# Optimization experiments

Measured on AMD Instinct MI355X. Metric: run time of the kernel, lower is better.

The kernel has to match this reference:

```python
import jax, jax.numpy as jnp
import numpy as np

VOCAB = 50257
D_MODEL = 256
HIDDEN = 512
NUM_CLASSES = 2
BATCH = 64
SEQ = 512
PAD_IDX = 0


def setup_inputs() -> dict:
    key = jax.random.key(0)
    ks = jax.random.split(key, 8)
    input_ids = jax.random.randint(ks[0], (BATCH, SEQ), 0, VOCAB)
    emb = jax.random.normal(ks[1], (VOCAB, D_MODEL), dtype=jnp.float32) * 0.02
    emb = emb.at[PAD_IDX].set(0.0)  # padding_idx row is zero
    s_x = 1.0 / np.sqrt(D_MODEL)
    s_h = 1.0 / np.sqrt(HIDDEN)
    Wx = jax.random.uniform(ks[2], (D_MODEL, 3 * HIDDEN), minval=-s_x, maxval=s_x)
    Wh = jax.random.uniform(ks[3], (HIDDEN, 3 * HIDDEN), minval=-s_h, maxval=s_h)
    bx = jax.random.uniform(ks[4], (3 * HIDDEN,), minval=-s_h, maxval=s_h)
    bh = jax.random.uniform(ks[5], (3 * HIDDEN,), minval=-s_h, maxval=s_h)
    Wo = jax.random.uniform(ks[6], (HIDDEN, NUM_CLASSES), minval=-s_h, maxval=s_h)
    bo = jax.random.uniform(ks[7], (NUM_CLASSES,), minval=-s_h, maxval=s_h)
    return {"input_ids": input_ids, "emb": emb, "Wx": Wx, "Wh": Wh,
            "bx": bx, "bh": bh, "Wo": Wo, "bo": bo}


def reference(input_ids, emb, Wx, Wh, bx, bh, Wo, bo):
    # Embedding lookup: [B, S, D]
    x = emb[input_ids]
    # Precompute input-side gate projections for all timesteps: [B, S, 3H]
    xg = jnp.einsum('bsd,dg->bsg', x, Wx) + bx
    H = Wh.shape[0]
    h0 = jnp.zeros((input_ids.shape[0], H), dtype=x.dtype)

    def step(h, xg_t):
        hg = h @ Wh + bh                    # [B, 3H]
        xr, xz, xn = jnp.split(xg_t, 3, axis=-1)
        hr, hz, hn = jnp.split(hg, 3, axis=-1)
        r = jax.nn.sigmoid(xr + hr)
        z = jax.nn.sigmoid(xz + hz)
        n = jnp.tanh(xn + r * hn)
        h_new = (1.0 - z) * n + z * h
        return h_new, None

    # scan over time; only the last hidden state feeds the classifier head
    h_last, _ = jax.lax.scan(step, h0, jnp.swapaxes(xg, 0, 1))
    # Dropout is identity in eval mode (p=0.5 at train time)
    logits = h_last @ Wo + bo               # [B, num_classes]
    return logits
```

## Files before the change

kernel.cpp:

```cpp
#include <hip/hip_runtime.h>
#include <hip/hip_bf16.h>

#define BATCH   64
#define SEQ     512
#define DMODEL  256
#define HIDDEN  512
#define G3      1536
#define NBLK    128
#define UPB     4
#define CPB     12
#define CHUNK   128
#define NCHUNK  4
#define HSLOT   (HIDDEN * BATCH)

typedef unsigned long long u64;
typedef unsigned int u32;

__global__ __launch_bounds__(512) void prep_wh(const float* __restrict__ Wh,
                                               float* __restrict__ whp) {
    int t = blockIdx.x * 512 + threadIdx.x;
    int k   = t & 511;
    int cb  = t >> 9;
    int c   = cb % 12;
    int blk = cb / 12;
    int u = c & 3, g = c >> 2;
    whp[t] = Wh[(long)k * G3 + g * HIDDEN + blk * UPB + u];
}

__global__ void init_flags(unsigned* flags) {
    __hip_atomic_store(&flags[threadIdx.x], 0u, __ATOMIC_RELAXED,
                       __HIP_MEMORY_SCOPE_AGENT);
}

__global__ __launch_bounds__(256) void xg_gemm(const int* __restrict__ ids,
                                               const float* __restrict__ emb,
                                               const float* __restrict__ Wx,
                                               const float* __restrict__ bx,
                                               float* __restrict__ xgC,
                                               int chunk) {
    __shared__ float Es[64][68];
    __shared__ float Ws[64][68];
    __shared__ int   sids[64];

    const int tid = threadIdx.x;
    const int nb = blockIdx.x;
    const int lt = blockIdx.y;
    const int s  = chunk * CHUNK + lt;
    const int tn = tid & 15;
    const int tm = tid >> 4;

    if (tid < 64) sids[tid] = ids[tid * SEQ + s];
    __syncthreads();

    float acc[4][4];
#pragma unroll
    for (int i = 0; i < 4; ++i)
#pragma unroll
        for (int j = 0; j < 4; ++j) acc[i][j] = 0.f;

    for (int kb = 0; kb < 256; kb += 64) {
#pragma unroll
        for (int p = 0; p < 4; ++p) {
            int b = p * 16 + tm;
            float4 av = *(const float4*)(emb + (long)sids[b] * DMODEL + kb + tn * 4);
            Es[tn * 4 + 0][b] = av.x;
            Es[tn * 4 + 1][b] = av.y;
            Es[tn * 4 + 2][b] = av.z;
            Es[tn * 4 + 3][b] = av.w;
            int krow = p * 16 + tm;
            float4 wv = *(const float4*)(Wx + (long)(kb + krow) * G3 + nb * 64 + tn * 4);
            *(float4*)&Ws[krow][tn * 4] = wv;
        }
        __syncthreads();
#pragma unroll
        for (int k = 0; k < 64; ++k) {
            float4 w4 = *(const float4*)&Ws[k][tm * 4];
            float4 e4 = *(const float4*)&Es[k][tn * 4];
            float ww[4] = {w4.x, w4.y, w4.z, w4.w};
            float ee[4] = {e4.x, e4.y, e4.z, e4.w};
#pragma unroll
            for (int i = 0; i < 4; ++i)
#pragma unroll
                for (int j = 0; j < 4; ++j)
                    acc[i][j] = fmaf(ww[i], ee[j], acc[i][j]);
        }
        __syncthreads();
    }

#pragma unroll
    for (int i = 0; i < 4; ++i) {
        int col = nb * 64 + tm * 4 + i;
        float bxi = bx[col];
        float4 o;
        o.x = acc[i][0] + bxi;
        o.y = acc[i][1] + bxi;
        o.z = acc[i][2] + bxi;
        o.w = acc[i][3] + bxi;
        *(float4*)(xgC + (long)col * (CHUNK * BATCH) + lt * 64 + tn * 4) = o;
    }
}

__global__ __launch_bounds__(512, 2) void gru_scan(const float* __restrict__ whp,
                                                   const float* __restrict__ xgC,
                                                   const float* __restrict__ bh,
                                                   float* hist,
                                                   unsigned* flags,
                                                   int chunk) {
    const int tid = threadIdx.x;
    const int blk = blockIdx.x;
    const int b   = tid & 63;
    const int wu  = __builtin_amdgcn_readfirstlane(tid >> 6);

    __shared__ float part[2][8][CPB][64];

    const float* wb = whp + blk * (CPB * HIDDEN) + wu * 64;
    const int base = chunk * CHUNK;

    int jg = 0;
    float bhr = 0.f, bhz = 0.f, bhn = 0.f, hprev = 0.f;
    const float* xr_p = nullptr; const float* xz_p = nullptr; const float* xn_p = nullptr;
    if (wu < 4) {
        jg  = blk * UPB + wu;
        bhr = bh[jg];
        bhz = bh[HIDDEN + jg];
        bhn = bh[2 * HIDDEN + jg];
        xr_p = xgC + (long)jg * (CHUNK * BATCH) + b;
        xz_p = xgC + (long)(HIDDEN + jg) * (CHUNK * BATCH) + b;
        xn_p = xgC + (long)(2 * HIDDEN + jg) * (CHUNK * BATCH) + b;
        hprev = (chunk == 0) ? 0.f : hist[(long)jg * 64 + b];
    }

#pragma unroll 1
    for (int lt = 0; lt < CHUNK; ++lt) {
        const int t  = base + lt;
        const int pb = lt & 1;
        const float* hs = hist + (long)lt * HSLOT;
        float*       hw = hist + (long)((lt + 1) & (CHUNK - 1)) * HSLOT;

        float xr = 0.f, xz = 0.f, xn = 0.f;
        if (wu < 4) {
            xr = xr_p[lt * 64];
            xz = xz_p[lt * 64];
            xn = xn_p[lt * 64];
        }

        float acc[CPB];
#pragma unroll
        for (int c = 0; c < CPB; ++c) acc[c] = 0.f;

        if (t > 0) {
            if (lt > 0) {
                const u32 tgt = (u32)t;
                for (;;) {
                    u32 f = __hip_atomic_load(&flags[wu * 64 + b], __ATOMIC_RELAXED,
                                              __HIP_MEMORY_SCOPE_AGENT);
                    if (__all((int)(f >= tgt))) break;
                    __builtin_amdgcn_s_sleep(1);
                }
            }
            const float* hq = hs + (long)wu * (64 * 64) + b;
            float hv[64];
#pragma unroll
            for (int i = 0; i < 64; ++i)
                hv[i] = hq[i * 64];

#pragma unroll
            for (int i = 0; i < 64; ++i) {
                const float hvv = hv[i];
#pragma unroll
                for (int c = 0; c < CPB; ++c)
                    acc[c] = fmaf(hvv, wb[c * HIDDEN + i], acc[c]);
            }
        }

#pragma unroll
        for (int c = 0; c < CPB; ++c) part[pb][wu][c][b] = acc[c];
        __syncthreads();

        if (wu < 4) {
            __builtin_amdgcn_s_setprio(1);
            float hgr = bhr, hgz = bhz, hgn = bhn;
#pragma unroll
            for (int ww = 0; ww < 8; ++ww) {
                hgr += part[pb][ww][wu][b];
                hgz += part[pb][ww][4 + wu][b];
                hgn += part[pb][ww][8 + wu][b];
            }
            float r  = 1.f / (1.f + expf(-(xr + hgr)));
            float z  = 1.f / (1.f + expf(-(xz + hgz)));
            float nn = tanhf(xn + r * hgn);
            float hnew = (1.f - z) * nn + z * hprev;
            hprev = hnew;
            __hip_atomic_store((u32*)hw + (long)jg * 64 + b, __float_as_uint(hnew),
                               __ATOMIC_RELAXED, __HIP_MEMORY_SCOPE_AGENT);
            asm volatile("s_waitcnt vmcnt(0)" ::: "memory");
            if (b == 0)
                __hip_atomic_store(&flags[jg], (u32)(t + 1), __ATOMIC_RELAXED,
                                   __HIP_MEMORY_SCOPE_AGENT);
            __builtin_amdgcn_s_setprio(0);
        }
    }
}

__global__ void head_kernel(const float* __restrict__ hist,
                            const float* __restrict__ Wo,
                            const float* __restrict__ bo,
                            float* __restrict__ out) {
    int tid = threadIdx.x;
    int b = tid >> 1, n = tid & 1;
    float acc = bo[n];
#pragma unroll 8
    for (int k = 0; k < HIDDEN; ++k)
        acc = fmaf(hist[(long)k * 64 + b], Wo[k * 2 + n], acc);
    out[b * 2 + n] = acc;
}

extern "C" void kernel_launch(void* const* d_in, const int* in_sizes, int n_in,
                              void* d_out, int out_size, void* d_ws, size_t ws_size,
                              hipStream_t stream) {
    (void)in_sizes; (void)n_in; (void)out_size; (void)ws_size;
    const int*   ids = (const int*)  d_in[0];
    const float* emb = (const float*)d_in[1];
    const float* Wx  = (const float*)d_in[2];
    const float* Wh  = (const float*)d_in[3];
    const float* bx  = (const float*)d_in[4];
    const float* bh  = (const float*)d_in[5];
    const float* Wo  = (const float*)d_in[6];
    const float* bo  = (const float*)d_in[7];
    float* out = (float*)d_out;

    char* ws = (char*)d_ws;
    unsigned* flags = (unsigned*)ws;
    float* hist = (float*)(ws + 2048);
    float* whp  = (float*)(ws + 2048 + (size_t)CHUNK * HSLOT * 4);
    float* xgC  = (float*)(ws + 2048 + (size_t)CHUNK * HSLOT * 4
                           + (size_t)NBLK * CPB * HIDDEN * 4);

    init_flags<<<dim3(1), dim3(512), 0, stream>>>(flags);
    prep_wh<<<dim3(1536), dim3(512), 0, stream>>>(Wh, whp);
    for (int c = 0; c < NCHUNK; ++c) {
        xg_gemm<<<dim3(24, CHUNK), dim3(256), 0, stream>>>(ids, emb, Wx, bx, xgC, c);
        gru_scan<<<dim3(NBLK), dim3(512), 0, stream>>>(whp, xgC, bh, hist, flags, c);
    }
    head_kernel<<<dim3(1), dim3(128), 0, stream>>>(hist, Wo, bo, out);
}
```

Measured before the change: 5.683 ms.

## Replace per-step flag handshake with NaN-sentinel polling on hidden-state data

Drops the separate flags array and the per-step store-wait-then-flag-publish protocol in the GRU scan. Consumers now poll the hidden-state slots directly with atomic loads until no value equals a NaN sentinel, and a new kernel refills the history buffer with sentinels before each chunk. This removes one dependent global-memory round trip per timestep from the serial critical path. In exchange it adds a 16 MB clear per chunk and busy-spinning full 64-value reloads without sleep, and it assumes the real hidden state never takes the sentinel bit pattern.

```diff
diff --git a/kernel.cpp b/kernel.cpp
--- a/kernel.cpp
+++ b/kernel.cpp
@@ -13,6 +13,9 @@
 #define NCHUNK  4
 #define HSLOT   (HIDDEN * BATCH)
 
+#define SENT32  0xFFC00000u
+#define SENT64  0xFFC00000FFC00000ULL
+
 typedef unsigned long long u64;
 typedef unsigned int u32;
 
@@ -27,9 +30,10 @@
     whp[t] = Wh[(long)k * G3 + g * HIDDEN + blk * UPB + u];
 }
 
-__global__ void init_flags(unsigned* flags) {
-    __hip_atomic_store(&flags[threadIdx.x], 0u, __ATOMIC_RELAXED,
-                       __HIP_MEMORY_SCOPE_AGENT);
+__global__ __launch_bounds__(256) void hist_clear(float* hist) {
+    long i = (long)blockIdx.x * 256 + threadIdx.x;
+    __hip_atomic_store((u64*)(hist + HSLOT) + i, SENT64,
+                       __ATOMIC_RELAXED, __HIP_MEMORY_SCOPE_AGENT);
 }
 
 __global__ __launch_bounds__(256) void xg_gemm(const int* __restrict__ ids,
@@ -104,7 +108,6 @@
                                                    const float* __restrict__ xgC,
                                                    const float* __restrict__ bh,
                                                    float* hist,
-                                                   unsigned* flags,
                                                    int chunk) {
     const int tid = threadIdx.x;
     const int blk = blockIdx.x;
@@ -134,8 +137,8 @@
     for (int lt = 0; lt < CHUNK; ++lt) {
         const int t  = base + lt;
         const int pb = lt & 1;
-        const float* hs = hist + (long)lt * HSLOT;
-        float*       hw = hist + (long)((lt + 1) & (CHUNK - 1)) * HSLOT;
+        const u32* hq = (const u32*)(hist + (long)lt * HSLOT) + wu * (64 * 64) + b;
+        float*     hw = hist + (long)((lt + 1) & (CHUNK - 1)) * HSLOT;
 
         float xr = 0.f, xz = 0.f, xn = 0.f;
         if (wu < 4) {
@@ -149,21 +152,18 @@
         for (int c = 0; c < CPB; ++c) acc[c] = 0.f;
 
         if (t > 0) {
-            if (lt > 0) {
-                const u32 tgt = (u32)t;
-                for (;;) {
-                    u32 f = __hip_atomic_load(&flags[wu * 64 + b], __ATOMIC_RELAXED,
+            float hv[64];
+            for (;;) {
+                int valid = 1;
+#pragma unroll
+                for (int i = 0; i < 64; ++i) {
+                    u32 w = __hip_atomic_load(hq + i * 64, __ATOMIC_RELAXED,
                                               __HIP_MEMORY_SCOPE_AGENT);
-                    if (__all((int)(f >= tgt))) break;
-                    __builtin_amdgcn_s_sleep(1);
+                    hv[i] = __uint_as_float(w);
+                    valid &= (w != SENT32);
                 }
+                if (__all(valid)) break;
             }
-            const float* hq = hs + (long)wu * (64 * 64) + b;
-            float hv[64];
-#pragma unroll
-            for (int i = 0; i < 64; ++i)
-                hv[i] = hq[i * 64];
-
 #pragma unroll
             for (int i = 0; i < 64; ++i) {
                 const float hvv = hv[i];
@@ -193,10 +193,6 @@
             hprev = hnew;
             __hip_atomic_store((u32*)hw + (long)jg * 64 + b, __float_as_uint(hnew),
                                __ATOMIC_RELAXED, __HIP_MEMORY_SCOPE_AGENT);
-            asm volatile("s_waitcnt vmcnt(0)" ::: "memory");
-            if (b == 0)
-                __hip_atomic_store(&flags[jg], (u32)(t + 1), __ATOMIC_RELAXED,
-                                   __HIP_MEMORY_SCOPE_AGENT);
             __builtin_amdgcn_s_setprio(0);
         }
     }
@@ -230,17 +226,16 @@
     float* out = (float*)d_out;
 
     char* ws = (char*)d_ws;
-    unsigned* flags = (unsigned*)ws;
-    float* hist = (float*)(ws + 2048);
-    float* whp  = (float*)(ws + 2048 + (size_t)CHUNK * HSLOT * 4);
-    float* xgC  = (float*)(ws + 2048 + (size_t)CHUNK * HSLOT * 4
+    float* hist = (float*)ws;
+    float* whp  = (float*)(ws + (size_t)CHUNK * HSLOT * 4);
+    float* xgC  = (float*)(ws + (size_t)CHUNK * HSLOT * 4
                            + (size_t)NBLK * CPB * HIDDEN * 4);
 
-    init_flags<<<dim3(1), dim3(512), 0, stream>>>(flags);
     prep_wh<<<dim3(1536), dim3(512), 0, stream>>>(Wh, whp);
     for (int c = 0; c < NCHUNK; ++c) {
+        hist_clear<<<dim3(8128), dim3(256), 0, stream>>>(hist);
         xg_gemm<<<dim3(24, CHUNK), dim3(256), 0, stream>>>(ids, emb, Wx, bx, xgC, c);
-        gru_scan<<<dim3(NBLK), dim3(512), 0, stream>>>(whp, xgC, bh, hist, flags, c);
+        gru_scan<<<dim3(NBLK), dim3(512), 0, stream>>>(whp, xgC, bh, hist, c);
     }
     head_kernel<<<dim3(1), dim3(128), 0, stream>>>(hist, Wo, bo, out);
 }
```

New measurement: 4.972 ms. 12.5% less time.
